# Kernel optimization log

Hardware: AMD Instinct MI355X
Metric: run time of the kernel (lower is better)

The kernel has to match this reference:

```python
import jax, jax.numpy as jnp
import numpy as np

COS_EPS = 1e-8  # torch F.cosine_similarity eps


def setup_inputs() -> dict:
    key = jax.random.key(0)
    k1, k2 = jax.random.split(key)
    x = jax.random.normal(k1, (8192, 512), dtype=jnp.float32)
    class_logits = jax.random.normal(k2, (8192, 100), dtype=jnp.float32)
    return {"x": x, "class_logits": class_logits}


def reference(x, class_logits):
    N, D = x.shape
    C = class_logits.shape[1]

    # class_logits.clone().detach()
    logits = jax.lax.stop_gradient(class_logits)
    pred = jax.nn.softmax(logits, axis=1)
    max_logit = pred.max(axis=1)          # [N]
    max_cls = pred.argmax(axis=1)         # [N] int

    # graph(): pairwise cosine similarity = normalize rows + gram matmul
    norms = jnp.linalg.norm(x, axis=1, keepdims=True)
    xn = x / jnp.maximum(norms, COS_EPS)
    mat = xn @ xn.T                       # [N, N]

    x_agg = mat @ x + x                   # [N, D]
    x_new = jax.lax.stop_gradient(x_agg)

    # update_prototype: per-class weighted scatter-add then mean over counts
    weighted = x_new * max_logit[:, None]                     # [N, D]
    sums = jax.ops.segment_sum(weighted, max_cls, num_segments=C)      # [C, D]
    counts = jax.ops.segment_sum(jnp.ones((N,), x.dtype), max_cls, num_segments=C)  # [C]
    prototypes = jnp.where(counts[:, None] > 0,
                           sums / jnp.maximum(counts, 1.0)[:, None],
                           jnp.zeros_like(sums))              # [C, D]

    # inter_class_matrix[i, j] = prototypes[j] - prototypes[i]
    inter_class_matrix = prototypes[None, :, :] - prototypes[:, None, :]  # [C, C, D]
    return prototypes, inter_class_matrix
```

## Files before the change

kernel.cpp:

```cpp
#include <hip/hip_runtime.h>
#include <math.h>

#define N_ROWS 8192
#define D_DIM  512
#define C_CLS  100

typedef unsigned short u16;
typedef unsigned int u32;
typedef __attribute__((ext_vector_type(8))) short short8;
typedef __attribute__((ext_vector_type(4))) float floatx4;

#define WS_G      0
#define WS_GP     262144
#define WS_INV    8650752
#define WS_WV     8658944
#define WS_CLS    8667136
#define WS_CNT    8675328
#define WS_OFFS   8675456
#define WS_CUR    8675584
#define WS_ORDER  8675712
#define WS_NTH    8683904
#define WS_NTL    10781056
#define WS_XTH    12878208
#define WS_XTL    14975360
#define WS_U      17072512
#define WS_V      17123712

__device__ __forceinline__ void split2(float v, u16& h, u16& l) {
    unsigned u = __float_as_uint(v);
    h = (u16)(u >> 16);
    float r = v - __uint_as_float(u & 0xFFFF0000u);
    l = (u16)(__float_as_uint(r) >> 16);
}

typedef const __attribute__((address_space(1))) u32* gp32;
typedef __attribute__((address_space(3))) u32* lp32;
__device__ __forceinline__ void cp16(const u16* g, u16* l) {
    __builtin_amdgcn_global_load_lds((gp32)g, (lp32)l, 16, 0, 0);
}

__global__ void k_softmax(const float* __restrict__ logits,
                          float* __restrict__ wv, int* __restrict__ cls,
                          int* __restrict__ cnt) {
    int wave = (blockIdx.x * blockDim.x + threadIdx.x) >> 6;
    int lane = threadIdx.x & 63;
    if (wave >= N_ROWS) return;
    const float* row = logits + (size_t)wave * C_CLS;
    float v1 = row[lane];
    bool has2 = (lane + 64) < C_CLS;
    float v2 = has2 ? row[lane + 64] : -INFINITY;
    float m; int idx;
    if (v2 > v1) { m = v2; idx = lane + 64; } else { m = v1; idx = lane; }
    #pragma unroll
    for (int off = 32; off >= 1; off >>= 1) {
        float om = __shfl_down(m, off);
        int   oi = __shfl_down(idx, off);
        if (om > m || (om == m && oi < idx)) { m = om; idx = oi; }
    }
    m = __shfl(m, 0);
    idx = __shfl(idx, 0);
    float s = expf(v1 - m) + (has2 ? expf(v2 - m) : 0.0f);
    #pragma unroll
    for (int off = 32; off >= 1; off >>= 1) s += __shfl_down(s, off);
    if (lane == 0) {
        wv[wave] = 1.0f / s;
        cls[wave] = idx;
        atomicAdd(&cnt[idx], 1);
    }
}

__global__ void k_norm(const float* __restrict__ x, float* __restrict__ inv) {
    int wave = (blockIdx.x * blockDim.x + threadIdx.x) >> 6;
    int lane = threadIdx.x & 63;
    if (wave >= N_ROWS) return;
    const float* row = x + (size_t)wave * D_DIM;
    float ss = 0.f;
    #pragma unroll
    for (int j = 0; j < D_DIM; j += 64) {
        float v = row[j + lane];
        ss += v * v;
    }
    #pragma unroll
    for (int off = 32; off >= 1; off >>= 1) ss += __shfl_down(ss, off);
    if (lane == 0) inv[wave] = 1.0f / fmaxf(sqrtf(ss), 1e-8f);
}

__global__ void k_scan(const int* __restrict__ cnt, int* __restrict__ offs) {
    __shared__ int s[128];
    int t = threadIdx.x;
    int v = (t < C_CLS) ? cnt[t] : 0;
    s[t] = v;
    __syncthreads();
    #pragma unroll
    for (int d = 1; d < 128; d <<= 1) {
        int add = (t >= d) ? s[t - d] : 0;
        __syncthreads();
        s[t] += add;
        __syncthreads();
    }
    if (t < C_CLS) offs[t] = s[t] - v;
}

__global__ void k_scatter(const int* __restrict__ cls, const int* __restrict__ offs,
                          int* __restrict__ cursor, int* __restrict__ order) {
    int m = blockIdx.x * 256 + threadIdx.x;
    int c = cls[m];
    int pos = atomicAdd(&cursor[c], 1);
    order[offs[c] + pos] = m;
}

#define LDT 65
__global__ __launch_bounds__(256) void k_convert(const float* __restrict__ x,
        const float* __restrict__ inv,
        u16* __restrict__ xth, u16* __restrict__ xtl,
        u16* __restrict__ nth, u16* __restrict__ ntl) {
    __shared__ unsigned xt_p[64 * LDT];
    __shared__ unsigned nt_p[64 * LDT];
    int r0 = blockIdx.x * 64, c0 = blockIdx.y * 64;
    int t = threadIdx.x;
    int r = t >> 2, cq = t & 3;
    const float* src = x + (size_t)(r0 + r) * D_DIM + c0 + cq * 16;
    float vv[16];
    {
        float4 a = *(const float4*)(src + 0);
        float4 b = *(const float4*)(src + 4);
        float4 c = *(const float4*)(src + 8);
        float4 d = *(const float4*)(src + 12);
        vv[0]=a.x; vv[1]=a.y; vv[2]=a.z; vv[3]=a.w;
        vv[4]=b.x; vv[5]=b.y; vv[6]=b.z; vv[7]=b.w;
        vv[8]=c.x; vv[9]=c.y; vv[10]=c.z; vv[11]=c.w;
        vv[12]=d.x; vv[13]=d.y; vv[14]=d.z; vv[15]=d.w;
    }
    float iv = inv[r0 + r];
    #pragma unroll
    for (int j = 0; j < 16; ++j) {
        u16 h, l, nh, nl;
        split2(vv[j], h, l);
        split2(iv * vv[j], nh, nl);
        int cl = cq * 16 + j;
        xt_p[cl * LDT + r] = ((unsigned)h  << 16) | l;
        nt_p[cl * LDT + r] = ((unsigned)nh << 16) | nl;
    }
    __syncthreads();
    int c = t >> 2, rq = (t & 3) * 16;
    size_t tbase = (size_t)(c0 + c) * N_ROWS + r0 + rq;
    {
        uint oh[8], ol[8];
        #pragma unroll
        for (int p = 0; p < 8; ++p) {
            unsigned d0 = xt_p[c * LDT + rq + 2*p];
            unsigned d1 = xt_p[c * LDT + rq + 2*p + 1];
            oh[p] = (d0 >> 16) | (d1 & 0xFFFF0000u);
            ol[p] = (d0 & 0xFFFFu) | (d1 << 16);
        }
        *(uint4*)&xth[tbase]     = make_uint4(oh[0], oh[1], oh[2], oh[3]);
        *(uint4*)&xth[tbase + 8] = make_uint4(oh[4], oh[5], oh[6], oh[7]);
        *(uint4*)&xtl[tbase]     = make_uint4(ol[0], ol[1], ol[2], ol[3]);
        *(uint4*)&xtl[tbase + 8] = make_uint4(ol[4], ol[5], ol[6], ol[7]);
    }
    {
        uint oh[8], ol[8];
        #pragma unroll
        for (int p = 0; p < 8; ++p) {
            unsigned d0 = nt_p[c * LDT + rq + 2*p];
            unsigned d1 = nt_p[c * LDT + rq + 2*p + 1];
            oh[p] = (d0 >> 16) | (d1 & 0xFFFF0000u);
            ol[p] = (d0 & 0xFFFFu) | (d1 << 16);
        }
        *(uint4*)&nth[tbase]     = make_uint4(oh[0], oh[1], oh[2], oh[3]);
        *(uint4*)&nth[tbase + 8] = make_uint4(oh[4], oh[5], oh[6], oh[7]);
        *(uint4*)&ntl[tbase]     = make_uint4(ol[0], ol[1], ol[2], ol[3]);
        *(uint4*)&ntl[tbase + 8] = make_uint4(ol[4], ol[5], ol[6], ol[7]);
    }
}

__global__ __launch_bounds__(256, 2) void k_gemm1(const u16* __restrict__ nth,
        const u16* __restrict__ ntl, const u16* __restrict__ xth,
        const u16* __restrict__ xtl, float* __restrict__ Gp) {
    __shared__ __attribute__((aligned(16))) u16 Ah[128*32], Al[128*32];
    __shared__ __attribute__((aligned(16))) u16 Bh[128*32], Bl[128*32];
    int i0 = (blockIdx.x & 3) << 7, j0 = (blockIdx.x >> 2) << 7;
    int kb = blockIdx.y << 8;
    int t = threadIdx.x, w = t >> 6, l = t & 63;
    int srow = t >> 2, scol = (t & 3) << 3;
    int lm = l & 15, lg = l >> 4;
    floatx4 acc[4][4];
    #pragma unroll
    for (int mi = 0; mi < 4; ++mi)
        #pragma unroll
        for (int ni = 0; ni < 4; ++ni) acc[mi][ni] = (floatx4){0.f,0.f,0.f,0.f};
    int d0 = srow * 32 + scol;
    int d1 = (64 + srow) * 32 + scol;
    const size_t ga0 = (size_t)(i0 + srow) * N_ROWS + kb + scol;
    const size_t ga1 = (size_t)(i0 + 64 + srow) * N_ROWS + kb + scol;
    const size_t gb0 = (size_t)(j0 + srow) * N_ROWS + kb + scol;
    const size_t gb1 = (size_t)(j0 + 64 + srow) * N_ROWS + kb + scol;
    for (int s = 0; s < 8; ++s) {
        int ks = s << 5;
        cp16(nth + ga0 + ks, Ah + d0);
        cp16(nth + ga1 + ks, Ah + d1);
        cp16(ntl + ga0 + ks, Al + d0);
        cp16(ntl + ga1 + ks, Al + d1);
        cp16(xth + gb0 + ks, Bh + d0);
        cp16(xth + gb1 + ks, Bh + d1);
        cp16(xtl + gb0 + ks, Bl + d0);
        cp16(xtl + gb1 + ks, Bl + d1);
        __syncthreads();
        short8 ah[4], al[4], bh[4], bl[4];
        #pragma unroll
        for (int mi = 0; mi < 4; ++mi) {
            int off = (((w & 1) << 6) + (mi << 4) + lm) * 32 + (lg << 3);
            ah[mi] = *(const short8*)&Ah[off];
            al[mi] = *(const short8*)&Al[off];
        }
        #pragma unroll
        for (int ni = 0; ni < 4; ++ni) {
            int off = (((w >> 1) << 6) + (ni << 4) + lm) * 32 + (lg << 3);
            bh[ni] = *(const short8*)&Bh[off];
            bl[ni] = *(const short8*)&Bl[off];
        }
        #pragma unroll
        for (int mi = 0; mi < 4; ++mi)
            #pragma unroll
            for (int ni = 0; ni < 4; ++ni) {
                acc[mi][ni] = __builtin_amdgcn_mfma_f32_16x16x32_bf16(ah[mi], bh[ni], acc[mi][ni], 0, 0, 0);
                acc[mi][ni] = __builtin_amdgcn_mfma_f32_16x16x32_bf16(ah[mi], bl[ni], acc[mi][ni], 0, 0, 0);
                acc[mi][ni] = __builtin_amdgcn_mfma_f32_16x16x32_bf16(al[mi], bh[ni], acc[mi][ni], 0, 0, 0);
            }
        __syncthreads();
    }
    float* Gb = Gp + ((size_t)blockIdx.y << 18);
    #pragma unroll
    for (int mi = 0; mi < 4; ++mi) {
        int row0 = i0 + ((w & 1) << 6) + (mi << 4) + (lg << 2);
        #pragma unroll
        for (int ni = 0; ni < 4; ++ni) {
            int col = j0 + ((w >> 1) << 6) + (ni << 4) + lm;
            #pragma unroll
            for (int r = 0; r < 4; ++r)
                Gb[(size_t)(row0 + r) * D_DIM + col] = acc[mi][ni][r];
        }
    }
}

__global__ void k_reduceG(const float* __restrict__ Gp, float* __restrict__ G) {
    int i = blockIdx.x * 256 + threadIdx.x;
    float s = 0.f;
    #pragma unroll
    for (int p = 0; p < 32; ++p) s += Gp[(size_t)p * (D_DIM * D_DIM) + i];
    G[i] = s;
}

__global__ __launch_bounds__(256) void k_uv(const float* __restrict__ x,
        const float* __restrict__ inv, const float* __restrict__ wv,
        const int* __restrict__ order, const int* __restrict__ offs,
        const int* __restrict__ cnt, float* __restrict__ u, float* __restrict__ v) {
    __shared__ float us[4][64], vs[4][64];
    int c = blockIdx.x, jc = blockIdx.y;
    int t = threadIdx.x, g = t >> 6, lane = t & 63;
    int j = jc * 64 + lane;
    int n = cnt[c], o = offs[c];
    float ua = 0.f, va = 0.f;
    for (int p = g; p < n; p += 4) {
        int m = order[o + p];
        float wm = wv[m];
        float wi = wm * inv[m];
        float xv = x[(size_t)m * D_DIM + j];
        ua += wi * xv; va += wm * xv;
    }
    us[g][lane] = ua; vs[g][lane] = va;
    __syncthreads();
    if (g == 0) {
        float uu = us[0][lane] + us[1][lane] + us[2][lane] + us[3][lane];
        float vv2 = vs[0][lane] + vs[1][lane] + vs[2][lane] + vs[3][lane];
        u[(size_t)c * D_DIM + j] = uu;
        v[(size_t)c * D_DIM + j] = vv2;
    }
}

__global__ __launch_bounds__(256) void k_pgemm(const float* __restrict__ u,
        const float* __restrict__ v, const int* __restrict__ cnt,
        const float* __restrict__ G, float* __restrict__ out) {
    __shared__ float us[D_DIM];
    int c = blockIdx.x >> 1;
    int j = ((blockIdx.x & 1) << 8) + threadIdx.x;
    us[threadIdx.x]       = u[(size_t)c * D_DIM + threadIdx.x];
    us[threadIdx.x + 256] = u[(size_t)c * D_DIM + threadIdx.x + 256];
    __syncthreads();
    float acc = v[(size_t)c * D_DIM + j];
    #pragma unroll 8
    for (int k = 0; k < D_DIM; ++k)
        acc += us[k] * G[(size_t)k * D_DIM + j];
    int n = cnt[c];
    float s = (n > 0) ? 1.0f / (float)n : 0.0f;
    out[(size_t)c * D_DIM + j] = acc * s;
}

__global__ void k_inter(const float* __restrict__ proto, float* __restrict__ out) {
    int pair = blockIdx.x;
    int i = pair / C_CLS;
    int j = pair - i * C_CLS;
    int d = threadIdx.x << 2;
    float4 pj = *(const float4*)&proto[j * D_DIM + d];
    float4 pi = *(const float4*)&proto[i * D_DIM + d];
    float4 r;
    r.x = pj.x - pi.x; r.y = pj.y - pi.y; r.z = pj.z - pi.z; r.w = pj.w - pi.w;
    *(float4*)&out[(size_t)pair * D_DIM + d] = r;
}

extern "C" void kernel_launch(void* const* d_in, const int* in_sizes, int n_in,
                              void* d_out, int out_size, void* d_ws, size_t ws_size,
                              hipStream_t stream) {
    const float* x      = (const float*)d_in[0];
    const float* logits = (const float*)d_in[1];
    float* out = (float*)d_out;
    float* ws  = (float*)d_ws;
    float* G     = ws + WS_G;
    float* Gp    = ws + WS_GP;
    float* inv   = ws + WS_INV;
    float* wv    = ws + WS_WV;
    int*   cls   = (int*)(ws + WS_CLS);
    int*   cnt   = (int*)(ws + WS_CNT);
    int*   offs  = (int*)(ws + WS_OFFS);
    int*   cur   = (int*)(ws + WS_CUR);
    int*   order = (int*)(ws + WS_ORDER);
    u16* nth = (u16*)(ws + WS_NTH);
    u16* ntl = (u16*)(ws + WS_NTL);
    u16* xth = (u16*)(ws + WS_XTH);
    u16* xtl = (u16*)(ws + WS_XTL);
    float* u_arr = ws + WS_U;
    float* v_arr = ws + WS_V;

    hipMemsetAsync((void*)cnt, 0, 384 * sizeof(int), stream);
    k_softmax<<<N_ROWS / 4, 256, 0, stream>>>(logits, wv, cls, cnt);
    k_norm<<<N_ROWS / 4, 256, 0, stream>>>(x, inv);
    k_scan<<<1, 128, 0, stream>>>(cnt, offs);
    k_scatter<<<N_ROWS / 256, 256, 0, stream>>>(cls, offs, cur, order);
    k_convert<<<dim3(128, 8), 256, 0, stream>>>(x, inv, xth, xtl, nth, ntl);
    k_gemm1<<<dim3(16, 32), 256, 0, stream>>>(nth, ntl, xth, xtl, Gp);
    k_reduceG<<<D_DIM * D_DIM / 256, 256, 0, stream>>>(Gp, G);
    k_uv<<<dim3(C_CLS, 8), 256, 0, stream>>>(x, inv, wv, order, offs, cnt, u_arr, v_arr);
    k_pgemm<<<C_CLS * 2, 256, 0, stream>>>(u_arr, v_arr, cnt, G, out);
    k_inter<<<C_CLS * C_CLS, 128, 0, stream>>>(out, out + C_CLS * D_DIM);
}
```

Before: 199.9 us.

## Symmetrize Gram via sqrt-inv scaling, compute upper tiles only, fuse small kernels

Rewrites the D×D Gram matrix X^T diag(inv) X as Z^T Z with Z = sqrt(inv)·X. This makes it symmetric, so only the 10 upper-triangular 128×128 tiles are computed and the diagonal tiles load a single operand. It removes one of the two transposed bf16 split copies and halves the conversion and GEMM load traffic. Softmax and norm are merged into one kernel, histogram/scan/scatter move into a spare block of the convert kernel, and the u/v class reduction runs as extra blocks of the GEMM launch, cutting launches and the memset. The risks are small numeric differences from the sqrt scaling and a serialized single-block sort running alongside conversion.

```diff
diff --git a/kernel.cpp b/kernel.cpp
--- a/kernel.cpp
+++ b/kernel.cpp
@@ -12,19 +12,17 @@
 
 #define WS_G      0
 #define WS_GP     262144
-#define WS_INV    8650752
-#define WS_WV     8658944
-#define WS_CLS    8667136
-#define WS_CNT    8675328
-#define WS_OFFS   8675456
-#define WS_CUR    8675584
-#define WS_ORDER  8675712
-#define WS_NTH    8683904
-#define WS_NTL    10781056
-#define WS_XTH    12878208
-#define WS_XTL    14975360
-#define WS_U      17072512
-#define WS_V      17123712
+#define WS_INV    5505024
+#define WS_SINV   5513216
+#define WS_WV     5521408
+#define WS_CLS    5529600
+#define WS_CNT    5537792
+#define WS_OFFS   5537920
+#define WS_ORDER  5538048
+#define WS_ZTH    5546240
+#define WS_ZTL    7643392
+#define WS_U      9740544
+#define WS_V      9791744
 
 __device__ __forceinline__ void split2(float v, u16& h, u16& l) {
     unsigned u = __float_as_uint(v);
@@ -39,9 +37,9 @@
     __builtin_amdgcn_global_load_lds((gp32)g, (lp32)l, 16, 0, 0);
 }
 
-__global__ void k_softmax(const float* __restrict__ logits,
-                          float* __restrict__ wv, int* __restrict__ cls,
-                          int* __restrict__ cnt) {
+__global__ __launch_bounds__(256) void k_prep(const float* __restrict__ logits,
+        const float* __restrict__ x, float* __restrict__ wv,
+        int* __restrict__ cls, float* __restrict__ inv, float* __restrict__ sinv) {
     int wave = (blockIdx.x * blockDim.x + threadIdx.x) >> 6;
     int lane = threadIdx.x & 63;
     if (wave >= N_ROWS) return;
@@ -62,62 +60,63 @@
     float s = expf(v1 - m) + (has2 ? expf(v2 - m) : 0.0f);
     #pragma unroll
     for (int off = 32; off >= 1; off >>= 1) s += __shfl_down(s, off);
+    const float* xr = x + (size_t)wave * D_DIM;
+    float ss = 0.f;
+    #pragma unroll
+    for (int j = 0; j < D_DIM; j += 64) {
+        float v = xr[j + lane];
+        ss += v * v;
+    }
+    #pragma unroll
+    for (int off = 32; off >= 1; off >>= 1) ss += __shfl_down(ss, off);
     if (lane == 0) {
         wv[wave] = 1.0f / s;
         cls[wave] = idx;
-        atomicAdd(&cnt[idx], 1);
-    }
-}
-
-__global__ void k_norm(const float* __restrict__ x, float* __restrict__ inv) {
-    int wave = (blockIdx.x * blockDim.x + threadIdx.x) >> 6;
-    int lane = threadIdx.x & 63;
-    if (wave >= N_ROWS) return;
-    const float* row = x + (size_t)wave * D_DIM;
-    float ss = 0.f;
-    #pragma unroll
-    for (int j = 0; j < D_DIM; j += 64) {
-        float v = row[j + lane];
-        ss += v * v;
-    }
-    #pragma unroll
-    for (int off = 32; off >= 1; off >>= 1) ss += __shfl_down(ss, off);
-    if (lane == 0) inv[wave] = 1.0f / fmaxf(sqrtf(ss), 1e-8f);
-}
-
-__global__ void k_scan(const int* __restrict__ cnt, int* __restrict__ offs) {
-    __shared__ int s[128];
+        float iv = 1.0f / fmaxf(sqrtf(ss), 1e-8f);
+        inv[wave] = iv;
+        sinv[wave] = sqrtf(iv);
+    }
+}
+
+#define LDT 65
+__global__ __launch_bounds__(256) void k_mid(const float* __restrict__ x,
+        const float* __restrict__ sinv, const int* __restrict__ cls,
+        u16* __restrict__ zth, u16* __restrict__ ztl,
+        int* __restrict__ cnt, int* __restrict__ offs, int* __restrict__ order) {
+    __shared__ unsigned zt_p[64 * LDT];
+    int bx = blockIdx.x;
     int t = threadIdx.x;
-    int v = (t < C_CLS) ? cnt[t] : 0;
-    s[t] = v;
-    __syncthreads();
-    #pragma unroll
-    for (int d = 1; d < 128; d <<= 1) {
-        int add = (t >= d) ? s[t - d] : 0;
-        __syncthreads();
-        s[t] += add;
-        __syncthreads();
-    }
-    if (t < C_CLS) offs[t] = s[t] - v;
-}
-
-__global__ void k_scatter(const int* __restrict__ cls, const int* __restrict__ offs,
-                          int* __restrict__ cursor, int* __restrict__ order) {
-    int m = blockIdx.x * 256 + threadIdx.x;
-    int c = cls[m];
-    int pos = atomicAdd(&cursor[c], 1);
-    order[offs[c] + pos] = m;
-}
-
-#define LDT 65
-__global__ __launch_bounds__(256) void k_convert(const float* __restrict__ x,
-        const float* __restrict__ inv,
-        u16* __restrict__ xth, u16* __restrict__ xtl,
-        u16* __restrict__ nth, u16* __restrict__ ntl) {
-    __shared__ unsigned xt_p[64 * LDT];
-    __shared__ unsigned nt_p[64 * LDT];
-    int r0 = blockIdx.x * 64, c0 = blockIdx.y * 64;
-    int t = threadIdx.x;
+    if (bx == 1024) {
+        __shared__ int hist[128], scan_s[128], cur[128];
+        if (t < 128) hist[t] = 0;
+        __syncthreads();
+        for (int m2 = t; m2 < N_ROWS; m2 += 256) atomicAdd(&hist[cls[m2]], 1);
+        __syncthreads();
+        if (t < 128) scan_s[t] = hist[t];
+        __syncthreads();
+        #pragma unroll
+        for (int d = 1; d < 128; d <<= 1) {
+            int add = 0;
+            if (t < 128 && t >= d) add = scan_s[t - d];
+            __syncthreads();
+            if (t < 128) scan_s[t] += add;
+            __syncthreads();
+        }
+        if (t < 128) {
+            int off0 = scan_s[t] - hist[t];
+            cur[t] = off0;
+            offs[t] = off0;
+            cnt[t] = hist[t];
+        }
+        __syncthreads();
+        for (int m2 = t; m2 < N_ROWS; m2 += 256) {
+            int c2 = cls[m2];
+            int p = atomicAdd(&cur[c2], 1);
+            order[p] = m2;
+        }
+        return;
+    }
+    int r0 = (bx & 127) << 6, c0 = (bx >> 7) << 6;
     int r = t >> 2, cq = t & 3;
     const float* src = x + (size_t)(r0 + r) * D_DIM + c0 + cq * 16;
     float vv[16];
@@ -131,57 +130,71 @@
         vv[8]=c.x; vv[9]=c.y; vv[10]=c.z; vv[11]=c.w;
         vv[12]=d.x; vv[13]=d.y; vv[14]=d.z; vv[15]=d.w;
     }
-    float iv = inv[r0 + r];
+    float sv = sinv[r0 + r];
     #pragma unroll
     for (int j = 0; j < 16; ++j) {
-        u16 h, l, nh, nl;
-        split2(vv[j], h, l);
-        split2(iv * vv[j], nh, nl);
-        int cl = cq * 16 + j;
-        xt_p[cl * LDT + r] = ((unsigned)h  << 16) | l;
-        nt_p[cl * LDT + r] = ((unsigned)nh << 16) | nl;
+        u16 h, l;
+        split2(sv * vv[j], h, l);
+        zt_p[(cq * 16 + j) * LDT + r] = ((unsigned)h << 16) | l;
     }
     __syncthreads();
     int c = t >> 2, rq = (t & 3) * 16;
     size_t tbase = (size_t)(c0 + c) * N_ROWS + r0 + rq;
-    {
-        uint oh[8], ol[8];
-        #pragma unroll
-        for (int p = 0; p < 8; ++p) {
-            unsigned d0 = xt_p[c * LDT + rq + 2*p];
-            unsigned d1 = xt_p[c * LDT + rq + 2*p + 1];
-            oh[p] = (d0 >> 16) | (d1 & 0xFFFF0000u);
-            ol[p] = (d0 & 0xFFFFu) | (d1 << 16);
-        }
-        *(uint4*)&xth[tbase]     = make_uint4(oh[0], oh[1], oh[2], oh[3]);
-        *(uint4*)&xth[tbase + 8] = make_uint4(oh[4], oh[5], oh[6], oh[7]);
-        *(uint4*)&xtl[tbase]     = make_uint4(ol[0], ol[1], ol[2], ol[3]);
-        *(uint4*)&xtl[tbase + 8] = make_uint4(ol[4], ol[5], ol[6], ol[7]);
-    }
-    {
-        uint oh[8], ol[8];
-        #pragma unroll
-        for (int p = 0; p < 8; ++p) {
-            unsigned d0 = nt_p[c * LDT + rq + 2*p];
-            unsigned d1 = nt_p[c * LDT + rq + 2*p + 1];
-            oh[p] = (d0 >> 16) | (d1 & 0xFFFF0000u);
-            ol[p] = (d0 & 0xFFFFu) | (d1 << 16);
-        }
-        *(uint4*)&nth[tbase]     = make_uint4(oh[0], oh[1], oh[2], oh[3]);
-        *(uint4*)&nth[tbase + 8] = make_uint4(oh[4], oh[5], oh[6], oh[7]);
-        *(uint4*)&ntl[tbase]     = make_uint4(ol[0], ol[1], ol[2], ol[3]);
-        *(uint4*)&ntl[tbase + 8] = make_uint4(ol[4], ol[5], ol[6], ol[7]);
-    }
-}
-
-__global__ __launch_bounds__(256, 2) void k_gemm1(const u16* __restrict__ nth,
-        const u16* __restrict__ ntl, const u16* __restrict__ xth,
-        const u16* __restrict__ xtl, float* __restrict__ Gp) {
+    uint oh[8], ol[8];
+    #pragma unroll
+    for (int p = 0; p < 8; ++p) {
+        unsigned d0 = zt_p[c * LDT + rq + 2*p];
+        unsigned d1 = zt_p[c * LDT + rq + 2*p + 1];
+        oh[p] = (d0 >> 16) | (d1 & 0xFFFF0000u);
+        ol[p] = (d0 & 0xFFFFu) | (d1 << 16);
+    }
+    *(uint4*)&zth[tbase]     = make_uint4(oh[0], oh[1], oh[2], oh[3]);
+    *(uint4*)&zth[tbase + 8] = make_uint4(oh[4], oh[5], oh[6], oh[7]);
+    *(uint4*)&ztl[tbase]     = make_uint4(ol[0], ol[1], ol[2], ol[3]);
+    *(uint4*)&ztl[tbase + 8] = make_uint4(ol[4], ol[5], ol[6], ol[7]);
+}
+
+__global__ __launch_bounds__(256) void k_big(const u16* __restrict__ zth,
+        const u16* __restrict__ ztl, const float* __restrict__ x,
+        const float* __restrict__ inv, const float* __restrict__ wv,
+        const int* __restrict__ order, const int* __restrict__ offs,
+        const int* __restrict__ cnt, float* __restrict__ Gp,
+        float* __restrict__ u, float* __restrict__ v) {
     __shared__ __attribute__((aligned(16))) u16 Ah[128*32], Al[128*32];
     __shared__ __attribute__((aligned(16))) u16 Bh[128*32], Bl[128*32];
-    int i0 = (blockIdx.x & 3) << 7, j0 = (blockIdx.x >> 2) << 7;
-    int kb = blockIdx.y << 8;
-    int t = threadIdx.x, w = t >> 6, l = t & 63;
+    __shared__ float us[4][64], vs[4][64];
+    int bx = blockIdx.x;
+    int t = threadIdx.x;
+    if (bx >= 320) {
+        int idx = bx - 320;
+        int c = idx >> 3, jc = idx & 7;
+        int g = t >> 6, lane = t & 63;
+        int j = jc * 64 + lane;
+        int n = cnt[c], o = offs[c];
+        float ua = 0.f, va = 0.f;
+        for (int p = g; p < n; p += 4) {
+            int m = order[o + p];
+            float wm = wv[m];
+            float wi = wm * inv[m];
+            float xv = x[(size_t)m * D_DIM + j];
+            ua += wi * xv; va += wm * xv;
+        }
+        us[g][lane] = ua; vs[g][lane] = va;
+        __syncthreads();
+        if (g == 0) {
+            u[(size_t)c * D_DIM + j] = us[0][lane] + us[1][lane] + us[2][lane] + us[3][lane];
+            v[(size_t)c * D_DIM + j] = vs[0][lane] + vs[1][lane] + vs[2][lane] + vs[3][lane];
+        }
+        return;
+    }
+    int tile = bx % 10;
+    int p = bx / 10;
+    int ti = tile < 4 ? 0 : (tile < 7 ? 1 : (tile < 9 ? 2 : 3));
+    int tj = tile - (ti == 0 ? 0 : (ti == 1 ? 3 : (ti == 2 ? 5 : 6)));
+    int i0 = ti << 7, j0 = tj << 7;
+    bool diag = (ti == tj);
+    int kb = p << 8;
+    int w = t >> 6, l = t & 63;
     int srow = t >> 2, scol = (t & 3) << 3;
     int lm = l & 15, lg = l >> 4;
     floatx4 acc[4][4];
@@ -195,16 +208,20 @@
     const size_t ga1 = (size_t)(i0 + 64 + srow) * N_ROWS + kb + scol;
     const size_t gb0 = (size_t)(j0 + srow) * N_ROWS + kb + scol;
     const size_t gb1 = (size_t)(j0 + 64 + srow) * N_ROWS + kb + scol;
+    const u16* Bhs = diag ? Ah : Bh;
+    const u16* Bls = diag ? Al : Bl;
     for (int s = 0; s < 8; ++s) {
         int ks = s << 5;
-        cp16(nth + ga0 + ks, Ah + d0);
-        cp16(nth + ga1 + ks, Ah + d1);
-        cp16(ntl + ga0 + ks, Al + d0);
-        cp16(ntl + ga1 + ks, Al + d1);
-        cp16(xth + gb0 + ks, Bh + d0);
-        cp16(xth + gb1 + ks, Bh + d1);
-        cp16(xtl + gb0 + ks, Bl + d0);
-        cp16(xtl + gb1 + ks, Bl + d1);
+        cp16(zth + ga0 + ks, Ah + d0);
+        cp16(zth + ga1 + ks, Ah + d1);
+        cp16(ztl + ga0 + ks, Al + d0);
+        cp16(ztl + ga1 + ks, Al + d1);
+        if (!diag) {
+            cp16(zth + gb0 + ks, Bh + d0);
+            cp16(zth + gb1 + ks, Bh + d1);
+            cp16(ztl + gb0 + ks, Bl + d0);
+            cp16(ztl + gb1 + ks, Bl + d1);
+        }
         __syncthreads();
         short8 ah[4], al[4], bh[4], bl[4];
         #pragma unroll
@@ -216,8 +233,8 @@
         #pragma unroll
         for (int ni = 0; ni < 4; ++ni) {
             int off = (((w >> 1) << 6) + (ni << 4) + lm) * 32 + (lg << 3);
-            bh[ni] = *(const short8*)&Bh[off];
-            bl[ni] = *(const short8*)&Bl[off];
+            bh[ni] = *(const short8*)&Bhs[off];
+            bl[ni] = *(const short8*)&Bls[off];
         }
         #pragma unroll
         for (int mi = 0; mi < 4; ++mi)
@@ -229,53 +246,31 @@
             }
         __syncthreads();
     }
-    float* Gb = Gp + ((size_t)blockIdx.y << 18);
+    float* Gb = Gp + ((size_t)(p * 10 + tile) << 14);
     #pragma unroll
     for (int mi = 0; mi < 4; ++mi) {
-        int row0 = i0 + ((w & 1) << 6) + (mi << 4) + (lg << 2);
+        int row0 = ((w & 1) << 6) + (mi << 4) + (lg << 2);
         #pragma unroll
         for (int ni = 0; ni < 4; ++ni) {
-            int col = j0 + ((w >> 1) << 6) + (ni << 4) + lm;
+            int col = ((w >> 1) << 6) + (ni << 4) + lm;
             #pragma unroll
             for (int r = 0; r < 4; ++r)
-                Gb[(size_t)(row0 + r) * D_DIM + col] = acc[mi][ni][r];
+                Gb[(size_t)(row0 + r) * 128 + col] = acc[mi][ni][r];
         }
     }
 }
 
 __global__ void k_reduceG(const float* __restrict__ Gp, float* __restrict__ G) {
     int i = blockIdx.x * 256 + threadIdx.x;
+    int r = i >> 9, c = i & 511;
+    int tr = r >> 7, tc = c >> 7, rr = r & 127, cc = c & 127;
+    if (tr > tc) { int tmp = tr; tr = tc; tc = tmp; tmp = rr; rr = cc; cc = tmp; }
+    int tid = tr * 4 + tc - ((tr * (tr + 1)) >> 1);
+    const float* src = Gp + ((size_t)tid << 14) + rr * 128 + cc;
     float s = 0.f;
     #pragma unroll
-    for (int p = 0; p < 32; ++p) s += Gp[(size_t)p * (D_DIM * D_DIM) + i];
+    for (int p = 0; p < 32; ++p) s += src[(size_t)p * 163840];
     G[i] = s;
-}
-
-__global__ __launch_bounds__(256) void k_uv(const float* __restrict__ x,
-        const float* __restrict__ inv, const float* __restrict__ wv,
-        const int* __restrict__ order, const int* __restrict__ offs,
-        const int* __restrict__ cnt, float* __restrict__ u, float* __restrict__ v) {
-    __shared__ float us[4][64], vs[4][64];
-    int c = blockIdx.x, jc = blockIdx.y;
-    int t = threadIdx.x, g = t >> 6, lane = t & 63;
-    int j = jc * 64 + lane;
-    int n = cnt[c], o = offs[c];
-    float ua = 0.f, va = 0.f;
-    for (int p = g; p < n; p += 4) {
-        int m = order[o + p];
-        float wm = wv[m];
-        float wi = wm * inv[m];
-        float xv = x[(size_t)m * D_DIM + j];
-        ua += wi * xv; va += wm * xv;
-    }
-    us[g][lane] = ua; vs[g][lane] = va;
-    __syncthreads();
-    if (g == 0) {
-        float uu = us[0][lane] + us[1][lane] + us[2][lane] + us[3][lane];
-        float vv2 = vs[0][lane] + vs[1][lane] + vs[2][lane] + vs[3][lane];
-        u[(size_t)c * D_DIM + j] = uu;
-        v[(size_t)c * D_DIM + j] = vv2;
-    }
 }
 
 __global__ __launch_bounds__(256) void k_pgemm(const float* __restrict__ u,
@@ -318,28 +313,21 @@
     float* G     = ws + WS_G;
     float* Gp    = ws + WS_GP;
     float* inv   = ws + WS_INV;
+    float* sinv  = ws + WS_SINV;
     float* wv    = ws + WS_WV;
     int*   cls   = (int*)(ws + WS_CLS);
     int*   cnt   = (int*)(ws + WS_CNT);
     int*   offs  = (int*)(ws + WS_OFFS);
-    int*   cur   = (int*)(ws + WS_CUR);
     int*   order = (int*)(ws + WS_ORDER);
-    u16* nth = (u16*)(ws + WS_NTH);
-    u16* ntl = (u16*)(ws + WS_NTL);
-    u16* xth = (u16*)(ws + WS_XTH);
-    u16* xtl = (u16*)(ws + WS_XTL);
+    u16* zth = (u16*)(ws + WS_ZTH);
+    u16* ztl = (u16*)(ws + WS_ZTL);
     float* u_arr = ws + WS_U;
     float* v_arr = ws + WS_V;
 
-    hipMemsetAsync((void*)cnt, 0, 384 * sizeof(int), stream);
-    k_softmax<<<N_ROWS / 4, 256, 0, stream>>>(logits, wv, cls, cnt);
-    k_norm<<<N_ROWS / 4, 256, 0, stream>>>(x, inv);
-    k_scan<<<1, 128, 0, stream>>>(cnt, offs);
-    k_scatter<<<N_ROWS / 256, 256, 0, stream>>>(cls, offs, cur, order);
-    k_convert<<<dim3(128, 8), 256, 0, stream>>>(x, inv, xth, xtl, nth, ntl);
-    k_gemm1<<<dim3(16, 32), 256, 0, stream>>>(nth, ntl, xth, xtl, Gp);
+    k_prep<<<N_ROWS / 4, 256, 0, stream>>>(logits, x, wv, cls, inv, sinv);
+    k_mid<<<1025, 256, 0, stream>>>(x, sinv, cls, zth, ztl, cnt, offs, order);
+    k_big<<<1120, 256, 0, stream>>>(zth, ztl, x, inv, wv, order, offs, cnt, Gp, u_arr, v_arr);
     k_reduceG<<<D_DIM * D_DIM / 256, 256, 0, stream>>>(Gp, G);
-    k_uv<<<dim3(C_CLS, 8), 256, 0, stream>>>(x, inv, wv, order, offs, cnt, u_arr, v_arr);
     k_pgemm<<<C_CLS * 2, 256, 0, stream>>>(u_arr, v_arr, cnt, G, out);
     k_inter<<<C_CLS * C_CLS, 128, 0, stream>>>(out, out + C_CLS * D_DIM);
 }
```

Result: faster. 178.8 us (-10.6%).
